# Optimization experiments

Hardware: AMD Instinct MI355X
Metric: run time of the kernel (lower is better)

Reference implementation:

```python
import jax, jax.numpy as jnp
import numpy as np

E = 1024
H = 16
HD = E // H


def setup_inputs() -> dict:
    key = jax.random.key(0)
    k1, k2, k3, k4, k5 = jax.random.split(key, 5)
    x = jax.random.normal(k1, (2, 2048, E), dtype=jnp.float32)
    s = 1.0 / np.sqrt(E)
    qkv_w = jax.random.uniform(k2, (3 * E, E), jnp.float32, -s, s)
    qkv_b = jax.random.uniform(k3, (3 * E,), jnp.float32, -s, s)
    o_w = jax.random.uniform(k4, (E, E), jnp.float32, -s, s)
    o_b = jax.random.uniform(k5, (E,), jnp.float32, -s, s)
    return {"x": x, "qkv_w": qkv_w, "qkv_b": qkv_b, "o_w": o_w, "o_b": o_b}


def reference(x, qkv_w, qkv_b, o_w, o_b):
    B, T, _ = x.shape
    # qkv projection (torch Linear: x @ W.T + b)
    qkv = x @ qkv_w.T + qkv_b  # [B,T,3E]
    q, k, v = jnp.split(qkv, 3, axis=-1)
    # [B,H,T,HD]
    q = q.reshape(B, T, H, HD).transpose(0, 2, 1, 3)
    k = k.reshape(B, T, H, HD).transpose(0, 2, 1, 3)
    v = v.reshape(B, T, H, HD).transpose(0, 2, 1, 3)
    scores = jnp.einsum('bhqd,bhkd->bhqk', q, k) / np.sqrt(HD)
    causal = jnp.tril(jnp.ones((T, T), dtype=bool))
    scores = jnp.where(causal, scores, -jnp.inf)
    attn = jax.nn.softmax(scores, axis=-1)  # dropout disabled (eval mode)
    y = jnp.einsum('bhqk,bhkd->bhqd', attn, v)
    y = y.transpose(0, 2, 1, 3).reshape(B, T, E)
    return y @ o_w.T + o_b
```

## Files before the change

### kernel.cpp

```cpp
#include <hip/hip_runtime.h>
#include <hip/hip_bf16.h>
#include <math.h>

#define BATCH 2
#define SEQ   2048
#define EMB   1024
#define NH    16
#define HD    64
#define M_ROWS (BATCH * SEQ)

typedef __attribute__((ext_vector_type(8))) short bf16x8;
typedef __attribute__((ext_vector_type(4))) float f32x4;

__device__ __forceinline__ ushort f2bf(float f) {
    unsigned u = __float_as_uint(f);
    unsigned lsb = (u >> 16) & 1u;
    u += 0x7fffu + lsb;
    return (ushort)(u >> 16);
}

__device__ __forceinline__ unsigned cvt_pk_bf16(float lo, float hi) {
    unsigned r;
    asm("v_cvt_pk_bf16_f32 %0, %1, %2" : "=v"(r) : "v"(lo), "v"(hi));
    return r;
}

__device__ __forceinline__ void gload_lds16(const void* g, void* l) {
    __builtin_amdgcn_global_load_lds(
        (const __attribute__((address_space(1))) unsigned int*)g,
        (__attribute__((address_space(3))) unsigned int*)l, 16, 0, 0);
}

__global__ __launch_bounds__(256) void cvt3_f32_bf16(
    const float* __restrict__ s1, const float* __restrict__ s2,
    const float* __restrict__ s3, ushort* __restrict__ out,
    int n1, int n2)
{
    int i = (blockIdx.x * 256 + threadIdx.x) * 4;
    const float* src;
    int off;
    if (i < n1)            { src = s1; off = i; }
    else if (i < n1 + n2)  { src = s2; off = i - n1; }
    else                   { src = s3; off = i - n1 - n2; }
    float4 v = *reinterpret_cast<const float4*>(&src[off]);
    uint2 pk;
    pk.x = cvt_pk_bf16(v.x, v.y);
    pk.y = cvt_pk_bf16(v.z, v.w);
    *reinterpret_cast<uint2*>(&out[i]) = pk;
}

template <int MODE>
__global__ __launch_bounds__(256) void gemm_mfma_abt(
    const ushort* __restrict__ A, const ushort* __restrict__ B,
    const float* __restrict__ bias, float* __restrict__ Cout,
    ushort* __restrict__ qkb, ushort* __restrict__ vtb,
    int M, int N, int K)
{
    __shared__ ushort Al[128 * 64];
    __shared__ ushort Bl[128 * 64];

    const int tid  = threadIdx.x;
    const int lane = tid & 63;
    const int wave = tid >> 6;
    const int wr   = wave >> 1;
    const int wc   = wave & 1;
    const int l15  = lane & 15;
    const int l4   = lane >> 4;
    const int m0   = blockIdx.y * 128;
    const int n0   = blockIdx.x * 128;

    f32x4 acc[4][4];
#pragma unroll
    for (int m = 0; m < 4; ++m)
#pragma unroll
        for (int n = 0; n < 4; ++n)
#pragma unroll
            for (int r = 0; r < 4; ++r) acc[m][n][r] = 0.f;

    for (int k0 = 0; k0 < K; k0 += 64) {
#pragma unroll
        for (int it = 0; it < 4; ++it) {
            int chunk = tid + it * 256;
            int row = chunk >> 3;
            int kc  = (chunk & 7) * 8;
            gload_lds16(&A[(size_t)(m0 + row) * K + k0 + kc], &Al[chunk * 8]);
            gload_lds16(&B[(size_t)(n0 + row) * K + k0 + kc], &Bl[chunk * 8]);
        }
        __syncthreads();

#pragma unroll
        for (int kk = 0; kk < 2; ++kk) {
            const int ko = kk * 32 + l4 * 8;
            bf16x8 a[4], b[4];
#pragma unroll
            for (int m = 0; m < 4; ++m)
                a[m] = *reinterpret_cast<const bf16x8*>(
                    &Al[(wr * 64 + m * 16 + l15) * 64 + ko]);
#pragma unroll
            for (int n = 0; n < 4; ++n)
                b[n] = *reinterpret_cast<const bf16x8*>(
                    &Bl[(wc * 64 + n * 16 + l15) * 64 + ko]);
            __builtin_amdgcn_s_setprio(1);
#pragma unroll
            for (int m = 0; m < 4; ++m)
#pragma unroll
                for (int n = 0; n < 4; ++n)
                    acc[m][n] = __builtin_amdgcn_mfma_f32_16x16x32_bf16(
                        a[m], b[n], acc[m][n], 0, 0, 0);
            __builtin_amdgcn_s_setprio(0);
        }
        __syncthreads();
    }

#pragma unroll
    for (int n = 0; n < 4; ++n) {
        const int col = n0 + wc * 64 + n * 16 + l15;
        const float bv = bias[col];
        if (MODE == 0) {
#pragma unroll
            for (int m = 0; m < 4; ++m) {
                const int row0 = m0 + wr * 64 + m * 16 + l4 * 4;
#pragma unroll
                for (int r = 0; r < 4; ++r)
                    Cout[(size_t)(row0 + r) * N + col] = acc[m][n][r] + bv;
            }
        } else if (col < 2 * EMB) {
#pragma unroll
            for (int m = 0; m < 4; ++m) {
                const int row0 = m0 + wr * 64 + m * 16 + l4 * 4;
#pragma unroll
                for (int r = 0; r < 4; ++r)
                    qkb[(size_t)(row0 + r) * 2048 + col] = f2bf(acc[m][n][r] + bv);
            }
        } else {
            const int h = (col - 2 * EMB) >> 6;
            const int d = col & 63;
#pragma unroll
            for (int m = 0; m < 4; ++m) {
                const int row0 = m0 + wr * 64 + m * 16 + l4 * 4;
                const int bb = row0 >> 11;
                const int t  = row0 & 2047;
                uint2 pk;
                pk.x = cvt_pk_bf16(acc[m][n][0] + bv, acc[m][n][1] + bv);
                pk.y = cvt_pk_bf16(acc[m][n][2] + bv, acc[m][n][3] + bv);
                *reinterpret_cast<uint2*>(
                    &vtb[((size_t)(bb * 16 + h) * 64 + d) * 2048 + t]) = pk;
            }
        }
    }
}

__global__ __launch_bounds__(256) void attn_mfma(
    const ushort* __restrict__ qk, const ushort* __restrict__ vt,
    ushort* __restrict__ y)
{
    __shared__ alignas(16) ushort Kl[4][4096];
    __shared__ alignas(16) ushort Vl[4][4096];
    __shared__ alignas(16) ushort QP[8192];

    const int tid  = threadIdx.x;
    const int lane = tid & 63;
    const int w    = tid >> 6;
    const int l15  = lane & 15;
    const int l4   = lane >> 4;

    const int id  = blockIdx.x;
    const int xcd = id & 7;
    const int s   = (id >> 3) & 15;
    const int g   = id >> 7;
    const int bh  = xcd * 4 + g;
    const int qt  = (g < 2) ? (15 - s) : s;
    const int b   = bh >> 4;
    const int h   = bh & 15;

    const ushort* qbase = qk + (size_t)b * SEQ * 2048 + h * HD;
    const ushort* kbase = qbase + EMB;
    const ushort* vbase = vt + (size_t)bh * HD * SEQ;

    const int swz   = (l15 & 7) << 4;
    const int koff0 = ((l4 * 16) ^ swz) >> 1;
    const int koff1 = ((64 + l4 * 16) ^ swz) >> 1;

#pragma unroll
    for (int it = 0; it < 4; ++it) {
        int i = tid + it * 256;
        int r = i >> 3;
        int c = ((i & 7) ^ (r & 7)) << 3;
        gload_lds16(qbase + (size_t)(qt * 128 + r) * 2048 + c, &QP[i * 8]);
    }
#pragma unroll
    for (int it = 0; it < 2; ++it) {
        int i = tid + it * 256;
        int r = i >> 3;
        int c = ((i & 7) ^ (r & 7)) << 3;
        gload_lds16(kbase + (size_t)r * 2048 + c, &Kl[0][i * 8]);
        gload_lds16(kbase + (size_t)(64 + r) * 2048 + c, &Kl[1][i * 8]);
    }
#pragma unroll
    for (int it = 0; it < 2; ++it) {
        int i = tid + it * 256;
        int d = i >> 3;
        int c = ((i & 7) ^ (d & 7)) << 3;
        gload_lds16(vbase + (size_t)d * 2048 + c, &Vl[0][i * 8]);
        gload_lds16(vbase + (size_t)d * 2048 + 64 + c, &Vl[1][i * 8]);
    }
    __syncthreads();

    const int qrow0 = (w * 32 + l15) * 64;
    const int qrow1 = (w * 32 + 16 + l15) * 64;
    const bf16x8 qf00 = *reinterpret_cast<const bf16x8*>(&QP[qrow0 + koff0]);
    const bf16x8 qf01 = *reinterpret_cast<const bf16x8*>(&QP[qrow0 + koff1]);
    const bf16x8 qf10 = *reinterpret_cast<const bf16x8*>(&QP[qrow1 + koff0]);
    const bf16x8 qf11 = *reinterpret_cast<const bf16x8*>(&QP[qrow1 + koff1]);

    int pso[4];
#pragma unroll
    for (int n = 0; n < 4; ++n) pso[n] = ((n * 32 + l4 * 8) ^ swz) >> 1;

    const short OBF = (short)0x3F80;
    const bf16x8 ones = {OBF, OBF, OBF, OBF, OBF, OBF, OBF, OBF};

    f32x4 o0[4], o1[4];
#pragma unroll
    for (int n = 0; n < 4; ++n)
#pragma unroll
        for (int r = 0; r < 4; ++r) { o0[n][r] = 0.f; o1[n][r] = 0.f; }
    f32x4 lacc0 = {0.f, 0.f, 0.f, 0.f};
    f32x4 lacc1 = {0.f, 0.f, 0.f, 0.f};
    float m0 = -3.0e38f;
    float m1 = -3.0e38f;

    const float BETA = 0.18033688f;
    const int nkv = 2 * qt + 2;

    auto computeTile = [&](const ushort* Kb, const ushort* Vb, int kkt) {
        bf16x8 kf[4][2];
#pragma unroll
        for (int n = 0; n < 4; ++n) {
            kf[n][0] = *reinterpret_cast<const bf16x8*>(
                &Kb[(n * 16 + l15) * 64 + koff0]);
            kf[n][1] = *reinterpret_cast<const bf16x8*>(
                &Kb[(n * 16 + l15) * 64 + koff1]);
        }
        f32x4 s0[4], s1[4];
        __builtin_amdgcn_s_setprio(1);
#pragma unroll
        for (int n = 0; n < 4; ++n) {
            f32x4 z0 = {0.f, 0.f, 0.f, 0.f};
            z0 = __builtin_amdgcn_mfma_f32_16x16x32_bf16(kf[n][0], qf00, z0, 0, 0, 0);
            s0[n] = __builtin_amdgcn_mfma_f32_16x16x32_bf16(kf[n][1], qf01, z0, 0, 0, 0);
            f32x4 z1 = {0.f, 0.f, 0.f, 0.f};
            z1 = __builtin_amdgcn_mfma_f32_16x16x32_bf16(kf[n][0], qf10, z1, 0, 0, 0);
            s1[n] = __builtin_amdgcn_mfma_f32_16x16x32_bf16(kf[n][1], qf11, z1, 0, 0, 0);
        }
        __builtin_amdgcn_s_setprio(0);

        bf16x8 vf[4][2];
#pragma unroll
        for (int n = 0; n < 4; ++n) {
            vf[n][0] = *reinterpret_cast<const bf16x8*>(
                &Vb[(n * 16 + l15) * 64 + koff0]);
            vf[n][1] = *reinterpret_cast<const bf16x8*>(
                &Vb[(n * 16 + l15) * 64 + koff1]);
        }

        if (kkt >= nkv - 2) {
            const int q0 = qt * 128 + w * 32 + l15;
            const int q1 = q0 + 16;
#pragma unroll
            for (int n = 0; n < 4; ++n)
#pragma unroll
                for (int r = 0; r < 4; ++r) {
                    int kg = kkt * 64 + n * 16 + l4 * 4 + r;
                    if (kg > q0) s0[n][r] = -3.0e38f;
                    if (kg > q1) s1[n][r] = -3.0e38f;
                }
        }

        float pm0, pm1;
        {
            float a0 = fmaxf(fmaxf(s0[0][0], s0[0][1]), fmaxf(s0[0][2], s0[0][3]));
            float a1 = fmaxf(fmaxf(s0[1][0], s0[1][1]), fmaxf(s0[1][2], s0[1][3]));
            float a2 = fmaxf(fmaxf(s0[2][0], s0[2][1]), fmaxf(s0[2][2], s0[2][3]));
            float a3 = fmaxf(fmaxf(s0[3][0], s0[3][1]), fmaxf(s0[3][2], s0[3][3]));
            pm0 = fmaxf(fmaxf(a0, a1), fmaxf(a2, a3)) * BETA;
            float b0 = fmaxf(fmaxf(s1[0][0], s1[0][1]), fmaxf(s1[0][2], s1[0][3]));
            float b1 = fmaxf(fmaxf(s1[1][0], s1[1][1]), fmaxf(s1[1][2], s1[1][3]));
            float b2 = fmaxf(fmaxf(s1[2][0], s1[2][1]), fmaxf(s1[2][2], s1[2][3]));
            float b3 = fmaxf(fmaxf(s1[3][0], s1[3][1]), fmaxf(s1[3][2], s1[3][3]));
            pm1 = fmaxf(fmaxf(b0, b1), fmaxf(b2, b3)) * BETA;
        }

        if (__any((pm0 > m0 + 8.0f) || (pm1 > m1 + 8.0f))) {
            float tm0 = fmaxf(pm0, __shfl_xor(pm0, 16));
            tm0 = fmaxf(tm0, __shfl_xor(tm0, 32));
            float tm1 = fmaxf(pm1, __shfl_xor(pm1, 16));
            tm1 = fmaxf(tm1, __shfl_xor(tm1, 32));
            float mn0 = fmaxf(m0, tm0);
            float al0 = exp2f(m0 - mn0);
            m0 = mn0;
            float mn1 = fmaxf(m1, tm1);
            float al1 = exp2f(m1 - mn1);
            m1 = mn1;
            float a00 = __shfl(al0, l4 * 4 + 0, 16);
            float a01 = __shfl(al0, l4 * 4 + 1, 16);
            float a02 = __shfl(al0, l4 * 4 + 2, 16);
            float a03 = __shfl(al0, l4 * 4 + 3, 16);
            float a10 = __shfl(al1, l4 * 4 + 0, 16);
            float a11 = __shfl(al1, l4 * 4 + 1, 16);
            float a12 = __shfl(al1, l4 * 4 + 2, 16);
            float a13 = __shfl(al1, l4 * 4 + 3, 16);
            lacc0[0] *= a00; lacc0[1] *= a01; lacc0[2] *= a02; lacc0[3] *= a03;
            lacc1[0] *= a10; lacc1[1] *= a11; lacc1[2] *= a12; lacc1[3] *= a13;
#pragma unroll
            for (int n = 0; n < 4; ++n) {
                o0[n][0] *= a00; o0[n][1] *= a01; o0[n][2] *= a02; o0[n][3] *= a03;
                o1[n][0] *= a10; o1[n][1] *= a11; o1[n][2] *= a12; o1[n][3] *= a13;
            }
        }

#pragma unroll
        for (int n = 0; n < 4; ++n) {
            float pa = exp2f(fmaf(s0[n][0], BETA, -m0));
            float pb = exp2f(fmaf(s0[n][1], BETA, -m0));
            float pc = exp2f(fmaf(s0[n][2], BETA, -m0));
            float pd = exp2f(fmaf(s0[n][3], BETA, -m0));
            uint2 pk;
            pk.x = cvt_pk_bf16(pa, pb);
            pk.y = cvt_pk_bf16(pc, pd);
            *reinterpret_cast<uint2*>(&QP[qrow0 + pso[n]]) = pk;
            pa = exp2f(fmaf(s1[n][0], BETA, -m1));
            pb = exp2f(fmaf(s1[n][1], BETA, -m1));
            pc = exp2f(fmaf(s1[n][2], BETA, -m1));
            pd = exp2f(fmaf(s1[n][3], BETA, -m1));
            pk.x = cvt_pk_bf16(pa, pb);
            pk.y = cvt_pk_bf16(pc, pd);
            *reinterpret_cast<uint2*>(&QP[qrow1 + pso[n]]) = pk;
        }

        bf16x8 pf00 = *reinterpret_cast<const bf16x8*>(&QP[qrow0 + koff0]);
        bf16x8 pf01 = *reinterpret_cast<const bf16x8*>(&QP[qrow0 + koff1]);
        bf16x8 pf10 = *reinterpret_cast<const bf16x8*>(&QP[qrow1 + koff0]);
        bf16x8 pf11 = *reinterpret_cast<const bf16x8*>(&QP[qrow1 + koff1]);
        __builtin_amdgcn_s_setprio(1);
        lacc0 = __builtin_amdgcn_mfma_f32_16x16x32_bf16(pf00, ones, lacc0, 0, 0, 0);
        lacc0 = __builtin_amdgcn_mfma_f32_16x16x32_bf16(pf01, ones, lacc0, 0, 0, 0);
        lacc1 = __builtin_amdgcn_mfma_f32_16x16x32_bf16(pf10, ones, lacc1, 0, 0, 0);
        lacc1 = __builtin_amdgcn_mfma_f32_16x16x32_bf16(pf11, ones, lacc1, 0, 0, 0);
#pragma unroll
        for (int n = 0; n < 4; ++n) {
            o0[n] = __builtin_amdgcn_mfma_f32_16x16x32_bf16(pf00, vf[n][0], o0[n], 0, 0, 0);
            o0[n] = __builtin_amdgcn_mfma_f32_16x16x32_bf16(pf01, vf[n][1], o0[n], 0, 0, 0);
            o1[n] = __builtin_amdgcn_mfma_f32_16x16x32_bf16(pf10, vf[n][0], o1[n], 0, 0, 0);
            o1[n] = __builtin_amdgcn_mfma_f32_16x16x32_bf16(pf11, vf[n][1], o1[n], 0, 0, 0);
        }
        __builtin_amdgcn_s_setprio(0);
    };

    for (int kk = 0; kk < nkv; kk += 2) {
        if (kk + 2 < nkv) {
            const int b2 = (kk + 2) & 3;
            const int b3 = (kk + 3) & 3;
#pragma unroll
            for (int it = 0; it < 2; ++it) {
                int i = tid + it * 256;
                int r = i >> 3;
                int c = ((i & 7) ^ (r & 7)) << 3;
                gload_lds16(kbase + (size_t)((kk + 2) * 64 + r) * 2048 + c,
                            &Kl[b2][i * 8]);
                gload_lds16(kbase + (size_t)((kk + 3) * 64 + r) * 2048 + c,
                            &Kl[b3][i * 8]);
            }
#pragma unroll
            for (int it = 0; it < 2; ++it) {
                int i = tid + it * 256;
                int d = i >> 3;
                int c = ((i & 7) ^ (d & 7)) << 3;
                gload_lds16(vbase + (size_t)d * 2048 + (kk + 2) * 64 + c,
                            &Vl[b2][i * 8]);
                gload_lds16(vbase + (size_t)d * 2048 + (kk + 3) * 64 + c,
                            &Vl[b3][i * 8]);
            }
        }

        computeTile(Kl[kk & 3], Vl[kk & 3], kk);
        computeTile(Kl[(kk + 1) & 3], Vl[(kk + 1) & 3], kk + 1);
        __syncthreads();
    }

#pragma unroll
    for (int r = 0; r < 4; ++r) {
        float inv0 = 1.f / lacc0[r];
        float inv1 = 1.f / lacc1[r];
        int row0 = qt * 128 + w * 32 + l4 * 4 + r;
        int row1 = row0 + 16;
#pragma unroll
        for (int n = 0; n < 4; ++n) {
            y[(size_t)(b * SEQ + row0) * EMB + h * HD + n * 16 + l15] =
                f2bf(o0[n][r] * inv0);
            y[(size_t)(b * SEQ + row1) * EMB + h * HD + n * 16 + l15] =
                f2bf(o1[n][r] * inv1);
        }
    }
}

extern "C" void kernel_launch(void* const* d_in, const int* in_sizes, int n_in,
                              void* d_out, int out_size, void* d_ws, size_t ws_size,
                              hipStream_t stream)
{
    const float* x     = (const float*)d_in[0];
    const float* qkv_w = (const float*)d_in[1];
    const float* qkv_b = (const float*)d_in[2];
    const float* o_w   = (const float*)d_in[3];
    const float* o_b   = (const float*)d_in[4];
    float* out = (float*)d_out;

    ushort* xb    = (ushort*)d_ws;
    ushort* wqkvb = xb    + (size_t)M_ROWS * EMB;
    ushort* owb   = wqkvb + (size_t)3 * EMB * EMB;
    ushort* qkb   = owb   + (size_t)EMB * EMB;
    ushort* vtb   = qkb   + (size_t)M_ROWS * 2 * EMB;
    ushort* ybb   = vtb   + (size_t)32 * HD * SEQ;

    {
        int n1 = M_ROWS * EMB;
        int n2 = 3 * EMB * EMB;
        int ntot = n1 + n2 + EMB * EMB;
        cvt3_f32_bf16<<<ntot / 1024, 256, 0, stream>>>(
            x, qkv_w, o_w, xb, n1, n2);
    }

    {
        dim3 grid(3 * EMB / 128, M_ROWS / 128);
        gemm_mfma_abt<1><<<grid, 256, 0, stream>>>(
            xb, wqkvb, qkv_b, nullptr, qkb, vtb, M_ROWS, 3 * EMB, EMB);
    }

    {
        attn_mfma<<<512, 256, 0, stream>>>(qkb, vtb, ybb);
    }

    {
        dim3 grid(EMB / 128, M_ROWS / 128);
        gemm_mfma_abt<0><<<grid, 256, 0, stream>>>(
            ybb, owb, o_b, out, nullptr, nullptr, M_ROWS, EMB, EMB);
    }
}
```

Before: 129.2 us.

## Use 512-thread attention blocks that each process a paired light and heavy query tile

The attention kernel now launches 256 blocks of 512 threads instead of 512 blocks of 256. Each wave owns 16 query rows rather than 32, and each block runs two passes over query tiles pp and 15-pp, so every block does the same total causal work. The aim is to balance causal work across blocks and get more waves per block to hide latency. In exchange, each wave has half the MFMA work per K/V tile, the two passes run back to back, and block-wide barriers now span 8 waves.

```diff
diff --git a/kernel.cpp b/kernel.cpp
--- a/kernel.cpp
+++ b/kernel.cpp
@@ -150,7 +150,7 @@
     }
 }
 
-__global__ __launch_bounds__(256) void attn_mfma(
+__global__ __launch_bounds__(512) void attn_mfma(
     const ushort* __restrict__ qk, const ushort* __restrict__ vt,
     ushort* __restrict__ y)
 {
@@ -166,10 +166,8 @@
 
     const int id  = blockIdx.x;
     const int xcd = id & 7;
-    const int s   = (id >> 3) & 15;
-    const int g   = id >> 7;
-    const int bh  = xcd * 4 + g;
-    const int qt  = (g < 2) ? (15 - s) : s;
+    const int bh  = xcd * 4 + ((id >> 3) & 3);
+    const int pp  = id >> 5;
     const int b   = bh >> 4;
     const int h   = bh & 15;
 
@@ -181,226 +179,162 @@
     const int koff0 = ((l4 * 16) ^ swz) >> 1;
     const int koff1 = ((64 + l4 * 16) ^ swz) >> 1;
 
-#pragma unroll
-    for (int it = 0; it < 4; ++it) {
-        int i = tid + it * 256;
-        int r = i >> 3;
-        int c = ((i & 7) ^ (r & 7)) << 3;
-        gload_lds16(qbase + (size_t)(qt * 128 + r) * 2048 + c, &QP[i * 8]);
-    }
-#pragma unroll
-    for (int it = 0; it < 2; ++it) {
-        int i = tid + it * 256;
-        int r = i >> 3;
-        int c = ((i & 7) ^ (r & 7)) << 3;
-        gload_lds16(kbase + (size_t)r * 2048 + c, &Kl[0][i * 8]);
-        gload_lds16(kbase + (size_t)(64 + r) * 2048 + c, &Kl[1][i * 8]);
-    }
-#pragma unroll
-    for (int it = 0; it < 2; ++it) {
-        int i = tid + it * 256;
-        int d = i >> 3;
-        int c = ((i & 7) ^ (d & 7)) << 3;
-        gload_lds16(vbase + (size_t)d * 2048 + c, &Vl[0][i * 8]);
-        gload_lds16(vbase + (size_t)d * 2048 + 64 + c, &Vl[1][i * 8]);
-    }
-    __syncthreads();
-
-    const int qrow0 = (w * 32 + l15) * 64;
-    const int qrow1 = (w * 32 + 16 + l15) * 64;
-    const bf16x8 qf00 = *reinterpret_cast<const bf16x8*>(&QP[qrow0 + koff0]);
-    const bf16x8 qf01 = *reinterpret_cast<const bf16x8*>(&QP[qrow0 + koff1]);
-    const bf16x8 qf10 = *reinterpret_cast<const bf16x8*>(&QP[qrow1 + koff0]);
-    const bf16x8 qf11 = *reinterpret_cast<const bf16x8*>(&QP[qrow1 + koff1]);
-
     int pso[4];
 #pragma unroll
     for (int n = 0; n < 4; ++n) pso[n] = ((n * 32 + l4 * 8) ^ swz) >> 1;
 
     const short OBF = (short)0x3F80;
     const bf16x8 ones = {OBF, OBF, OBF, OBF, OBF, OBF, OBF, OBF};
-
-    f32x4 o0[4], o1[4];
-#pragma unroll
-    for (int n = 0; n < 4; ++n)
-#pragma unroll
-        for (int r = 0; r < 4; ++r) { o0[n][r] = 0.f; o1[n][r] = 0.f; }
-    f32x4 lacc0 = {0.f, 0.f, 0.f, 0.f};
-    f32x4 lacc1 = {0.f, 0.f, 0.f, 0.f};
-    float m0 = -3.0e38f;
-    float m1 = -3.0e38f;
-
     const float BETA = 0.18033688f;
-    const int nkv = 2 * qt + 2;
-
-    auto computeTile = [&](const ushort* Kb, const ushort* Vb, int kkt) {
-        bf16x8 kf[4][2];
-#pragma unroll
-        for (int n = 0; n < 4; ++n) {
-            kf[n][0] = *reinterpret_cast<const bf16x8*>(
-                &Kb[(n * 16 + l15) * 64 + koff0]);
-            kf[n][1] = *reinterpret_cast<const bf16x8*>(
-                &Kb[(n * 16 + l15) * 64 + koff1]);
-        }
-        f32x4 s0[4], s1[4];
-        __builtin_amdgcn_s_setprio(1);
-#pragma unroll
-        for (int n = 0; n < 4; ++n) {
-            f32x4 z0 = {0.f, 0.f, 0.f, 0.f};
-            z0 = __builtin_amdgcn_mfma_f32_16x16x32_bf16(kf[n][0], qf00, z0, 0, 0, 0);
-            s0[n] = __builtin_amdgcn_mfma_f32_16x16x32_bf16(kf[n][1], qf01, z0, 0, 0, 0);
-            f32x4 z1 = {0.f, 0.f, 0.f, 0.f};
-            z1 = __builtin_amdgcn_mfma_f32_16x16x32_bf16(kf[n][0], qf10, z1, 0, 0, 0);
-            s1[n] = __builtin_amdgcn_mfma_f32_16x16x32_bf16(kf[n][1], qf11, z1, 0, 0, 0);
-        }
-        __builtin_amdgcn_s_setprio(0);
-
-        bf16x8 vf[4][2];
-#pragma unroll
-        for (int n = 0; n < 4; ++n) {
-            vf[n][0] = *reinterpret_cast<const bf16x8*>(
-                &Vb[(n * 16 + l15) * 64 + koff0]);
-            vf[n][1] = *reinterpret_cast<const bf16x8*>(
-                &Vb[(n * 16 + l15) * 64 + koff1]);
-        }
-
-        if (kkt >= nkv - 2) {
-            const int q0 = qt * 128 + w * 32 + l15;
-            const int q1 = q0 + 16;
-#pragma unroll
-            for (int n = 0; n < 4; ++n)
-#pragma unroll
-                for (int r = 0; r < 4; ++r) {
-                    int kg = kkt * 64 + n * 16 + l4 * 4 + r;
-                    if (kg > q0) s0[n][r] = -3.0e38f;
-                    if (kg > q1) s1[n][r] = -3.0e38f;
+
+    const int qrow = (w * 16 + l15) * 64;
+
+    const int sr = tid >> 3;
+    const int sc = ((tid & 7) ^ (sr & 7)) << 3;
+    const int i2 = tid + 512;
+    const int qr2 = i2 >> 3;
+    const int qc2 = ((i2 & 7) ^ (qr2 & 7)) << 3;
+
+#pragma unroll
+    for (int pass = 0; pass < 2; ++pass) {
+        const int qt  = pass ? (15 - pp) : pp;
+        const int nkv = 2 * qt + 2;
+
+        gload_lds16(qbase + (size_t)(qt * 128 + sr) * 2048 + sc, &QP[tid * 8]);
+        gload_lds16(qbase + (size_t)(qt * 128 + qr2) * 2048 + qc2, &QP[i2 * 8]);
+        gload_lds16(kbase + (size_t)sr * 2048 + sc, &Kl[0][tid * 8]);
+        gload_lds16(kbase + (size_t)(64 + sr) * 2048 + sc, &Kl[1][tid * 8]);
+        gload_lds16(vbase + (size_t)sr * 2048 + sc, &Vl[0][tid * 8]);
+        gload_lds16(vbase + (size_t)sr * 2048 + 64 + sc, &Vl[1][tid * 8]);
+        __syncthreads();
+
+        const bf16x8 qf0 = *reinterpret_cast<const bf16x8*>(&QP[qrow + koff0]);
+        const bf16x8 qf1 = *reinterpret_cast<const bf16x8*>(&QP[qrow + koff1]);
+
+        f32x4 o[4];
+#pragma unroll
+        for (int n = 0; n < 4; ++n)
+#pragma unroll
+            for (int r = 0; r < 4; ++r) o[n][r] = 0.f;
+        f32x4 lacc = {0.f, 0.f, 0.f, 0.f};
+        float m = -3.0e38f;
+
+        auto computeTile = [&](const ushort* Kb, const ushort* Vb, int kkt) {
+            bf16x8 kf[4][2];
+#pragma unroll
+            for (int n = 0; n < 4; ++n) {
+                kf[n][0] = *reinterpret_cast<const bf16x8*>(
+                    &Kb[(n * 16 + l15) * 64 + koff0]);
+                kf[n][1] = *reinterpret_cast<const bf16x8*>(
+                    &Kb[(n * 16 + l15) * 64 + koff1]);
+            }
+            f32x4 s[4];
+            __builtin_amdgcn_s_setprio(1);
+#pragma unroll
+            for (int n = 0; n < 4; ++n) {
+                f32x4 z = {0.f, 0.f, 0.f, 0.f};
+                z = __builtin_amdgcn_mfma_f32_16x16x32_bf16(kf[n][0], qf0, z, 0, 0, 0);
+                s[n] = __builtin_amdgcn_mfma_f32_16x16x32_bf16(kf[n][1], qf1, z, 0, 0, 0);
+            }
+            __builtin_amdgcn_s_setprio(0);
+
+            bf16x8 vf[4][2];
+#pragma unroll
+            for (int n = 0; n < 4; ++n) {
+                vf[n][0] = *reinterpret_cast<const bf16x8*>(
+                    &Vb[(n * 16 + l15) * 64 + koff0]);
+                vf[n][1] = *reinterpret_cast<const bf16x8*>(
+                    &Vb[(n * 16 + l15) * 64 + koff1]);
+            }
+
+            if (kkt >= nkv - 2) {
+                const int q0 = qt * 128 + w * 16 + l15;
+#pragma unroll
+                for (int n = 0; n < 4; ++n)
+#pragma unroll
+                    for (int r = 0; r < 4; ++r) {
+                        int kg = kkt * 64 + n * 16 + l4 * 4 + r;
+                        if (kg > q0) s[n][r] = -3.0e38f;
+                    }
+            }
+
+            float a0 = fmaxf(fmaxf(s[0][0], s[0][1]), fmaxf(s[0][2], s[0][3]));
+            float a1 = fmaxf(fmaxf(s[1][0], s[1][1]), fmaxf(s[1][2], s[1][3]));
+            float a2 = fmaxf(fmaxf(s[2][0], s[2][1]), fmaxf(s[2][2], s[2][3]));
+            float a3 = fmaxf(fmaxf(s[3][0], s[3][1]), fmaxf(s[3][2], s[3][3]));
+            float pm = fmaxf(fmaxf(a0, a1), fmaxf(a2, a3)) * BETA;
+
+            if (__any(pm > m + 8.0f)) {
+                float tm = fmaxf(pm, __shfl_xor(pm, 16));
+                tm = fmaxf(tm, __shfl_xor(tm, 32));
+                float mn = fmaxf(m, tm);
+                float al = exp2f(m - mn);
+                m = mn;
+                float b0 = __shfl(al, l4 * 4 + 0, 16);
+                float b1 = __shfl(al, l4 * 4 + 1, 16);
+                float b2 = __shfl(al, l4 * 4 + 2, 16);
+                float b3 = __shfl(al, l4 * 4 + 3, 16);
+                lacc[0] *= b0; lacc[1] *= b1; lacc[2] *= b2; lacc[3] *= b3;
+#pragma unroll
+                for (int n = 0; n < 4; ++n) {
+                    o[n][0] *= b0; o[n][1] *= b1; o[n][2] *= b2; o[n][3] *= b3;
                 }
-        }
-
-        float pm0, pm1;
-        {
-            float a0 = fmaxf(fmaxf(s0[0][0], s0[0][1]), fmaxf(s0[0][2], s0[0][3]));
-            float a1 = fmaxf(fmaxf(s0[1][0], s0[1][1]), fmaxf(s0[1][2], s0[1][3]));
-            float a2 = fmaxf(fmaxf(s0[2][0], s0[2][1]), fmaxf(s0[2][2], s0[2][3]));
-            float a3 = fmaxf(fmaxf(s0[3][0], s0[3][1]), fmaxf(s0[3][2], s0[3][3]));
-            pm0 = fmaxf(fmaxf(a0, a1), fmaxf(a2, a3)) * BETA;
-            float b0 = fmaxf(fmaxf(s1[0][0], s1[0][1]), fmaxf(s1[0][2], s1[0][3]));
-            float b1 = fmaxf(fmaxf(s1[1][0], s1[1][1]), fmaxf(s1[1][2], s1[1][3]));
-            float b2 = fmaxf(fmaxf(s1[2][0], s1[2][1]), fmaxf(s1[2][2], s1[2][3]));
-            float b3 = fmaxf(fmaxf(s1[3][0], s1[3][1]), fmaxf(s1[3][2], s1[3][3]));
-            pm1 = fmaxf(fmaxf(b0, b1), fmaxf(b2, b3)) * BETA;
-        }
-
-        if (__any((pm0 > m0 + 8.0f) || (pm1 > m1 + 8.0f))) {
-            float tm0 = fmaxf(pm0, __shfl_xor(pm0, 16));
-            tm0 = fmaxf(tm0, __shfl_xor(tm0, 32));
-            float tm1 = fmaxf(pm1, __shfl_xor(pm1, 16));
-            tm1 = fmaxf(tm1, __shfl_xor(tm1, 32));
-            float mn0 = fmaxf(m0, tm0);
-            float al0 = exp2f(m0 - mn0);
-            m0 = mn0;
-            float mn1 = fmaxf(m1, tm1);
-            float al1 = exp2f(m1 - mn1);
-            m1 = mn1;
-            float a00 = __shfl(al0, l4 * 4 + 0, 16);
-            float a01 = __shfl(al0, l4 * 4 + 1, 16);
-            float a02 = __shfl(al0, l4 * 4 + 2, 16);
-            float a03 = __shfl(al0, l4 * 4 + 3, 16);
-            float a10 = __shfl(al1, l4 * 4 + 0, 16);
-            float a11 = __shfl(al1, l4 * 4 + 1, 16);
-            float a12 = __shfl(al1, l4 * 4 + 2, 16);
-            float a13 = __shfl(al1, l4 * 4 + 3, 16);
-            lacc0[0] *= a00; lacc0[1] *= a01; lacc0[2] *= a02; lacc0[3] *= a03;
-            lacc1[0] *= a10; lacc1[1] *= a11; lacc1[2] *= a12; lacc1[3] *= a13;
-#pragma unroll
-            for (int n = 0; n < 4; ++n) {
-                o0[n][0] *= a00; o0[n][1] *= a01; o0[n][2] *= a02; o0[n][3] *= a03;
-                o1[n][0] *= a10; o1[n][1] *= a11; o1[n][2] *= a12; o1[n][3] *= a13;
-            }
-        }
-
-#pragma unroll
-        for (int n = 0; n < 4; ++n) {
-            float pa = exp2f(fmaf(s0[n][0], BETA, -m0));
-            float pb = exp2f(fmaf(s0[n][1], BETA, -m0));
-            float pc = exp2f(fmaf(s0[n][2], BETA, -m0));
-            float pd = exp2f(fmaf(s0[n][3], BETA, -m0));
-            uint2 pk;
-            pk.x = cvt_pk_bf16(pa, pb);
-            pk.y = cvt_pk_bf16(pc, pd);
-            *reinterpret_cast<uint2*>(&QP[qrow0 + pso[n]]) = pk;
-            pa = exp2f(fmaf(s1[n][0], BETA, -m1));
-            pb = exp2f(fmaf(s1[n][1], BETA, -m1));
-            pc = exp2f(fmaf(s1[n][2], BETA, -m1));
-            pd = exp2f(fmaf(s1[n][3], BETA, -m1));
-            pk.x = cvt_pk_bf16(pa, pb);
-            pk.y = cvt_pk_bf16(pc, pd);
-            *reinterpret_cast<uint2*>(&QP[qrow1 + pso[n]]) = pk;
-        }
-
-        bf16x8 pf00 = *reinterpret_cast<const bf16x8*>(&QP[qrow0 + koff0]);
-        bf16x8 pf01 = *reinterpret_cast<const bf16x8*>(&QP[qrow0 + koff1]);
-        bf16x8 pf10 = *reinterpret_cast<const bf16x8*>(&QP[qrow1 + koff0]);
-        bf16x8 pf11 = *reinterpret_cast<const bf16x8*>(&QP[qrow1 + koff1]);
-        __builtin_amdgcn_s_setprio(1);
-        lacc0 = __builtin_amdgcn_mfma_f32_16x16x32_bf16(pf00, ones, lacc0, 0, 0, 0);
-        lacc0 = __builtin_amdgcn_mfma_f32_16x16x32_bf16(pf01, ones, lacc0, 0, 0, 0);
-        lacc1 = __builtin_amdgcn_mfma_f32_16x16x32_bf16(pf10, ones, lacc1, 0, 0, 0);
-        lacc1 = __builtin_amdgcn_mfma_f32_16x16x32_bf16(pf11, ones, lacc1, 0, 0, 0);
-#pragma unroll
-        for (int n = 0; n < 4; ++n) {
-            o0[n] = __builtin_amdgcn_mfma_f32_16x16x32_bf16(pf00, vf[n][0], o0[n], 0, 0, 0);
-            o0[n] = __builtin_amdgcn_mfma_f32_16x16x32_bf16(pf01, vf[n][1], o0[n], 0, 0, 0);
-            o1[n] = __builtin_amdgcn_mfma_f32_16x16x32_bf16(pf10, vf[n][0], o1[n], 0, 0, 0);
-            o1[n] = __builtin_amdgcn_mfma_f32_16x16x32_bf16(pf11, vf[n][1], o1[n], 0, 0, 0);
-        }
-        __builtin_amdgcn_s_setprio(0);
-    };
-
-    for (int kk = 0; kk < nkv; kk += 2) {
-        if (kk + 2 < nkv) {
-            const int b2 = (kk + 2) & 3;
-            const int b3 = (kk + 3) & 3;
-#pragma unroll
-            for (int it = 0; it < 2; ++it) {
-                int i = tid + it * 256;
-                int r = i >> 3;
-                int c = ((i & 7) ^ (r & 7)) << 3;
-                gload_lds16(kbase + (size_t)((kk + 2) * 64 + r) * 2048 + c,
-                            &Kl[b2][i * 8]);
-                gload_lds16(kbase + (size_t)((kk + 3) * 64 + r) * 2048 + c,
-                            &Kl[b3][i * 8]);
-            }
-#pragma unroll
-            for (int it = 0; it < 2; ++it) {
-                int i = tid + it * 256;
-                int d = i >> 3;
-                int c = ((i & 7) ^ (d & 7)) << 3;
-                gload_lds16(vbase + (size_t)d * 2048 + (kk + 2) * 64 + c,
-                            &Vl[b2][i * 8]);
-                gload_lds16(vbase + (size_t)d * 2048 + (kk + 3) * 64 + c,
-                            &Vl[b3][i * 8]);
-            }
-        }
-
-        computeTile(Kl[kk & 3], Vl[kk & 3], kk);
-        computeTile(Kl[(kk + 1) & 3], Vl[(kk + 1) & 3], kk + 1);
+            }
+
+#pragma unroll
+            for (int n = 0; n < 4; ++n) {
+                float pa = exp2f(fmaf(s[n][0], BETA, -m));
+                float pb = exp2f(fmaf(s[n][1], BETA, -m));
+                float pc = exp2f(fmaf(s[n][2], BETA, -m));
+                float pd = exp2f(fmaf(s[n][3], BETA, -m));
+                uint2 pk;
+                pk.x = cvt_pk_bf16(pa, pb);
+                pk.y = cvt_pk_bf16(pc, pd);
+                *reinterpret_cast<uint2*>(&QP[qrow + pso[n]]) = pk;
+            }
+
+            bf16x8 pf0 = *reinterpret_cast<const bf16x8*>(&QP[qrow + koff0]);
+            bf16x8 pf1 = *reinterpret_cast<const bf16x8*>(&QP[qrow + koff1]);
+            __builtin_amdgcn_s_setprio(1);
+            lacc = __builtin_amdgcn_mfma_f32_16x16x32_bf16(pf0, ones, lacc, 0, 0, 0);
+            lacc = __builtin_amdgcn_mfma_f32_16x16x32_bf16(pf1, ones, lacc, 0, 0, 0);
+#pragma unroll
+            for (int n = 0; n < 4; ++n) {
+                o[n] = __builtin_amdgcn_mfma_f32_16x16x32_bf16(pf0, vf[n][0], o[n], 0, 0, 0);
+                o[n] = __builtin_amdgcn_mfma_f32_16x16x32_bf16(pf1, vf[n][1], o[n], 0, 0, 0);
+            }
+            __builtin_amdgcn_s_setprio(0);
+        };
+
+        for (int kk = 0; kk < nkv; kk += 2) {
+            if (kk + 2 < nkv) {
+                const int b2 = (kk + 2) & 3;
+                const int b3 = (kk + 3) & 3;
+                gload_lds16(kbase + (size_t)((kk + 2) * 64 + sr) * 2048 + sc,
+                            &Kl[b2][tid * 8]);
+                gload_lds16(kbase + (size_t)((kk + 3) * 64 + sr) * 2048 + sc,
+                            &Kl[b3][tid * 8]);
+                gload_lds16(vbase + (size_t)sr * 2048 + (kk + 2) * 64 + sc,
+                            &Vl[b2][tid * 8]);
+                gload_lds16(vbase + (size_t)sr * 2048 + (kk + 3) * 64 + sc,
+                            &Vl[b3][tid * 8]);
+            }
+            computeTile(Kl[kk & 3], Vl[kk & 3], kk);
+            computeTile(Kl[(kk + 1) & 3], Vl[(kk + 1) & 3], kk + 1);
+            __syncthreads();
+        }
+
+#pragma unroll
+        for (int r = 0; r < 4; ++r) {
+            float inv = 1.f / lacc[r];
+            int row = qt * 128 + w * 16 + l4 * 4 + r;
+#pragma unroll
+            for (int n = 0; n < 4; ++n) {
+                y[(size_t)(b * SEQ + row) * EMB + h * HD + n * 16 + l15] =
+                    f2bf(o[n][r] * inv);
+            }
+        }
         __syncthreads();
-    }
-
-#pragma unroll
-    for (int r = 0; r < 4; ++r) {
-        float inv0 = 1.f / lacc0[r];
-        float inv1 = 1.f / lacc1[r];
-        int row0 = qt * 128 + w * 32 + l4 * 4 + r;
-        int row1 = row0 + 16;
-#pragma unroll
-        for (int n = 0; n < 4; ++n) {
-            y[(size_t)(b * SEQ + row0) * EMB + h * HD + n * 16 + l15] =
-                f2bf(o0[n][r] * inv0);
-            y[(size_t)(b * SEQ + row1) * EMB + h * HD + n * 16 + l15] =
-                f2bf(o1[n][r] * inv1);
-        }
     }
 }
 
@@ -437,7 +371,7 @@
     }
 
     {
-        attn_mfma<<<512, 256, 0, stream>>>(qkb, vtb, ybb);
+        attn_mfma<<<256, 512, 0, stream>>>(qkb, vtb, ybb);
     }
 
     {
```

After: 113.7 us. -12.0%, faster.

## Pair mirrored causal query tiles in one block sharing K/V loads, prescale Q

Applied to the files above, without the earlier changes.

The attention kernel now runs 512-thread blocks where two groups of four waves handle a query tile and its mirrored partner (pp and 15-pp). Both groups share the same K/V LDS stream, so each K/V tile is loaded once for two query tiles and every block has balanced causal work. Waves skip tiles beyond their causal limit, including the last half tile for some waves. The softmax scale (1/sqrt(d)·log2e) is folded into Q in the QKV GEMM epilogue, which removes per-element FMAs in the inner loop. The trade-offs are one extra bf16 rounding on the scaled Q, half as many blocks in the grid, and idle waves in the diagonal tiles.

```diff
diff --git a/kernel.cpp b/kernel.cpp
--- a/kernel.cpp
+++ b/kernel.cpp
@@ -125,12 +125,14 @@
                     Cout[(size_t)(row0 + r) * N + col] = acc[m][n][r] + bv;
             }
         } else if (col < 2 * EMB) {
+            const float qs = (col < EMB) ? 0.18033688f : 1.0f;
 #pragma unroll
             for (int m = 0; m < 4; ++m) {
                 const int row0 = m0 + wr * 64 + m * 16 + l4 * 4;
 #pragma unroll
                 for (int r = 0; r < 4; ++r)
-                    qkb[(size_t)(row0 + r) * 2048 + col] = f2bf(acc[m][n][r] + bv);
+                    qkb[(size_t)(row0 + r) * 2048 + col] =
+                        f2bf((acc[m][n][r] + bv) * qs);
             }
         } else {
             const int h = (col - 2 * EMB) >> 6;
@@ -150,28 +152,32 @@
     }
 }
 
-__global__ __launch_bounds__(256) void attn_mfma(
+__global__ __launch_bounds__(512) void attn_mfma(
     const ushort* __restrict__ qk, const ushort* __restrict__ vt,
     ushort* __restrict__ y)
 {
     __shared__ alignas(16) ushort Kl[4][4096];
     __shared__ alignas(16) ushort Vl[4][4096];
-    __shared__ alignas(16) ushort QP[8192];
+    __shared__ alignas(16) ushort QP[16384];
 
     const int tid  = threadIdx.x;
     const int lane = tid & 63;
     const int w    = tid >> 6;
+    const int u    = w & 3;
+    const int wg   = w >> 2;
     const int l15  = lane & 15;
     const int l4   = lane >> 4;
 
     const int id  = blockIdx.x;
     const int xcd = id & 7;
-    const int s   = (id >> 3) & 15;
-    const int g   = id >> 7;
-    const int bh  = xcd * 4 + g;
-    const int qt  = (g < 2) ? (15 - s) : s;
+    const int bh  = xcd * 4 + ((id >> 3) & 3);
+    const int pp  = id >> 5;
     const int b   = bh >> 4;
     const int h   = bh & 15;
+
+    const int qtX  = wg ? (15 - pp) : pp;
+    const int nkvX = 2 * qtX + 2;
+    const int nkvM = 32 - 2 * pp;
 
     const ushort* qbase = qk + (size_t)b * SEQ * 2048 + h * HD;
     const ushort* kbase = qbase + EMB;
@@ -180,46 +186,38 @@
     const int swz   = (l15 & 7) << 4;
     const int koff0 = ((l4 * 16) ^ swz) >> 1;
     const int koff1 = ((64 + l4 * 16) ^ swz) >> 1;
+    int pso[4];
+#pragma unroll
+    for (int n = 0; n < 4; ++n) pso[n] = ((n * 32 + l4 * 8) ^ swz) >> 1;
+
+    const short OBF = (short)0x3F80;
+    const bf16x8 ones = {OBF, OBF, OBF, OBF, OBF, OBF, OBF, OBF};
+
+    const int qrow0 = (wg * 128 + u * 32 + l15) * 64;
+    const int qrow1 = qrow0 + 16 * 64;
+
+    const int sr = tid >> 3;
+    const int sc = ((tid & 7) ^ (sr & 7)) << 3;
 
 #pragma unroll
     for (int it = 0; it < 4; ++it) {
-        int i = tid + it * 256;
-        int r = i >> 3;
-        int c = ((i & 7) ^ (r & 7)) << 3;
-        gload_lds16(qbase + (size_t)(qt * 128 + r) * 2048 + c, &QP[i * 8]);
-    }
-#pragma unroll
-    for (int it = 0; it < 2; ++it) {
-        int i = tid + it * 256;
-        int r = i >> 3;
-        int c = ((i & 7) ^ (r & 7)) << 3;
-        gload_lds16(kbase + (size_t)r * 2048 + c, &Kl[0][i * 8]);
-        gload_lds16(kbase + (size_t)(64 + r) * 2048 + c, &Kl[1][i * 8]);
-    }
-#pragma unroll
-    for (int it = 0; it < 2; ++it) {
-        int i = tid + it * 256;
-        int d = i >> 3;
-        int c = ((i & 7) ^ (d & 7)) << 3;
-        gload_lds16(vbase + (size_t)d * 2048 + c, &Vl[0][i * 8]);
-        gload_lds16(vbase + (size_t)d * 2048 + 64 + c, &Vl[1][i * 8]);
-    }
+        int c = tid + it * 512;
+        int r256 = c >> 3;
+        int cc = ((c & 7) ^ (r256 & 7)) << 3;
+        int grow = ((r256 >> 7) ? (15 - pp) : pp) * 128 + (r256 & 127);
+        gload_lds16(qbase + (size_t)grow * 2048 + cc, &QP[c * 8]);
+    }
+    gload_lds16(kbase + (size_t)sr * 2048 + sc, &Kl[0][tid * 8]);
+    gload_lds16(kbase + (size_t)(64 + sr) * 2048 + sc, &Kl[1][tid * 8]);
+    gload_lds16(vbase + (size_t)sr * 2048 + sc, &Vl[0][tid * 8]);
+    gload_lds16(vbase + (size_t)sr * 2048 + 64 + sc, &Vl[1][tid * 8]);
     __syncthreads();
 
-    const int qrow0 = (w * 32 + l15) * 64;
-    const int qrow1 = (w * 32 + 16 + l15) * 64;
     const bf16x8 qf00 = *reinterpret_cast<const bf16x8*>(&QP[qrow0 + koff0]);
     const bf16x8 qf01 = *reinterpret_cast<const bf16x8*>(&QP[qrow0 + koff1]);
     const bf16x8 qf10 = *reinterpret_cast<const bf16x8*>(&QP[qrow1 + koff0]);
     const bf16x8 qf11 = *reinterpret_cast<const bf16x8*>(&QP[qrow1 + koff1]);
 
-    int pso[4];
-#pragma unroll
-    for (int n = 0; n < 4; ++n) pso[n] = ((n * 32 + l4 * 8) ^ swz) >> 1;
-
-    const short OBF = (short)0x3F80;
-    const bf16x8 ones = {OBF, OBF, OBF, OBF, OBF, OBF, OBF, OBF};
-
     f32x4 o0[4], o1[4];
 #pragma unroll
     for (int n = 0; n < 4; ++n)
@@ -227,11 +225,10 @@
         for (int r = 0; r < 4; ++r) { o0[n][r] = 0.f; o1[n][r] = 0.f; }
     f32x4 lacc0 = {0.f, 0.f, 0.f, 0.f};
     f32x4 lacc1 = {0.f, 0.f, 0.f, 0.f};
-    float m0 = -3.0e38f;
-    float m1 = -3.0e38f;
-
-    const float BETA = 0.18033688f;
-    const int nkv = 2 * qt + 2;
+    float m0 = -3.0e38f, m1 = -3.0e38f;
+
+    const int q0g = qtX * 128 + u * 32 + l15;
+    const int q1g = q0g + 16;
 
     auto computeTile = [&](const ushort* Kb, const ushort* Vb, int kkt) {
         bf16x8 kf[4][2];
@@ -264,32 +261,27 @@
                 &Vb[(n * 16 + l15) * 64 + koff1]);
         }
 
-        if (kkt >= nkv - 2) {
-            const int q0 = qt * 128 + w * 32 + l15;
-            const int q1 = q0 + 16;
+        if (kkt >= nkvX - 2) {
 #pragma unroll
             for (int n = 0; n < 4; ++n)
 #pragma unroll
                 for (int r = 0; r < 4; ++r) {
                     int kg = kkt * 64 + n * 16 + l4 * 4 + r;
-                    if (kg > q0) s0[n][r] = -3.0e38f;
-                    if (kg > q1) s1[n][r] = -3.0e38f;
+                    if (kg > q0g) s0[n][r] = -3.0e38f;
+                    if (kg > q1g) s1[n][r] = -3.0e38f;
                 }
         }
 
-        float pm0, pm1;
-        {
-            float a0 = fmaxf(fmaxf(s0[0][0], s0[0][1]), fmaxf(s0[0][2], s0[0][3]));
-            float a1 = fmaxf(fmaxf(s0[1][0], s0[1][1]), fmaxf(s0[1][2], s0[1][3]));
-            float a2 = fmaxf(fmaxf(s0[2][0], s0[2][1]), fmaxf(s0[2][2], s0[2][3]));
-            float a3 = fmaxf(fmaxf(s0[3][0], s0[3][1]), fmaxf(s0[3][2], s0[3][3]));
-            pm0 = fmaxf(fmaxf(a0, a1), fmaxf(a2, a3)) * BETA;
-            float b0 = fmaxf(fmaxf(s1[0][0], s1[0][1]), fmaxf(s1[0][2], s1[0][3]));
-            float b1 = fmaxf(fmaxf(s1[1][0], s1[1][1]), fmaxf(s1[1][2], s1[1][3]));
-            float b2 = fmaxf(fmaxf(s1[2][0], s1[2][1]), fmaxf(s1[2][2], s1[2][3]));
-            float b3 = fmaxf(fmaxf(s1[3][0], s1[3][1]), fmaxf(s1[3][2], s1[3][3]));
-            pm1 = fmaxf(fmaxf(b0, b1), fmaxf(b2, b3)) * BETA;
-        }
+        float pa0 = fmaxf(fmaxf(s0[0][0], s0[0][1]), fmaxf(s0[0][2], s0[0][3]));
+        float pa1 = fmaxf(fmaxf(s0[1][0], s0[1][1]), fmaxf(s0[1][2], s0[1][3]));
+        float pa2 = fmaxf(fmaxf(s0[2][0], s0[2][1]), fmaxf(s0[2][2], s0[2][3]));
+        float pa3 = fmaxf(fmaxf(s0[3][0], s0[3][1]), fmaxf(s0[3][2], s0[3][3]));
+        float pm0 = fmaxf(fmaxf(pa0, pa1), fmaxf(pa2, pa3));
+        float pb0 = fmaxf(fmaxf(s1[0][0], s1[0][1]), fmaxf(s1[0][2], s1[0][3]));
+        float pb1 = fmaxf(fmaxf(s1[1][0], s1[1][1]), fmaxf(s1[1][2], s1[1][3]));
+        float pb2 = fmaxf(fmaxf(s1[2][0], s1[2][1]), fmaxf(s1[2][2], s1[2][3]));
+        float pb3 = fmaxf(fmaxf(s1[3][0], s1[3][1]), fmaxf(s1[3][2], s1[3][3]));
+        float pm1 = fmaxf(fmaxf(pb0, pb1), fmaxf(pb2, pb3));
 
         if (__any((pm0 > m0 + 8.0f) || (pm1 > m1 + 8.0f))) {
             float tm0 = fmaxf(pm0, __shfl_xor(pm0, 16));
@@ -321,18 +313,18 @@
 
 #pragma unroll
         for (int n = 0; n < 4; ++n) {
-            float pa = exp2f(fmaf(s0[n][0], BETA, -m0));
-            float pb = exp2f(fmaf(s0[n][1], BETA, -m0));
-            float pc = exp2f(fmaf(s0[n][2], BETA, -m0));
-            float pd = exp2f(fmaf(s0[n][3], BETA, -m0));
+            float pa = exp2f(s0[n][0] - m0);
+            float pb = exp2f(s0[n][1] - m0);
+            float pc = exp2f(s0[n][2] - m0);
+            float pd = exp2f(s0[n][3] - m0);
             uint2 pk;
             pk.x = cvt_pk_bf16(pa, pb);
             pk.y = cvt_pk_bf16(pc, pd);
             *reinterpret_cast<uint2*>(&QP[qrow0 + pso[n]]) = pk;
-            pa = exp2f(fmaf(s1[n][0], BETA, -m1));
-            pb = exp2f(fmaf(s1[n][1], BETA, -m1));
-            pc = exp2f(fmaf(s1[n][2], BETA, -m1));
-            pd = exp2f(fmaf(s1[n][3], BETA, -m1));
+            pa = exp2f(s1[n][0] - m1);
+            pb = exp2f(s1[n][1] - m1);
+            pc = exp2f(s1[n][2] - m1);
+            pd = exp2f(s1[n][3] - m1);
             pk.x = cvt_pk_bf16(pa, pb);
             pk.y = cvt_pk_bf16(pc, pd);
             *reinterpret_cast<uint2*>(&QP[qrow1 + pso[n]]) = pk;
@@ -357,34 +349,27 @@
         __builtin_amdgcn_s_setprio(0);
     };
 
-    for (int kk = 0; kk < nkv; kk += 2) {
-        if (kk + 2 < nkv) {
+    auto doTile = [&](int t) {
+        if (t >= nkvX) return;
+        if (t == nkvX - 1 && u < 2) return;
+        computeTile(Kl[t & 3], Vl[t & 3], t);
+    };
+
+    for (int kk = 0; kk < nkvM; kk += 2) {
+        if (kk + 2 < nkvM) {
             const int b2 = (kk + 2) & 3;
             const int b3 = (kk + 3) & 3;
-#pragma unroll
-            for (int it = 0; it < 2; ++it) {
-                int i = tid + it * 256;
-                int r = i >> 3;
-                int c = ((i & 7) ^ (r & 7)) << 3;
-                gload_lds16(kbase + (size_t)((kk + 2) * 64 + r) * 2048 + c,
-                            &Kl[b2][i * 8]);
-                gload_lds16(kbase + (size_t)((kk + 3) * 64 + r) * 2048 + c,
-                            &Kl[b3][i * 8]);
-            }
-#pragma unroll
-            for (int it = 0; it < 2; ++it) {
-                int i = tid + it * 256;
-                int d = i >> 3;
-                int c = ((i & 7) ^ (d & 7)) << 3;
-                gload_lds16(vbase + (size_t)d * 2048 + (kk + 2) * 64 + c,
-                            &Vl[b2][i * 8]);
-                gload_lds16(vbase + (size_t)d * 2048 + (kk + 3) * 64 + c,
-                            &Vl[b3][i * 8]);
-            }
-        }
-
-        computeTile(Kl[kk & 3], Vl[kk & 3], kk);
-        computeTile(Kl[(kk + 1) & 3], Vl[(kk + 1) & 3], kk + 1);
+            gload_lds16(kbase + (size_t)((kk + 2) * 64 + sr) * 2048 + sc,
+                        &Kl[b2][tid * 8]);
+            gload_lds16(kbase + (size_t)((kk + 3) * 64 + sr) * 2048 + sc,
+                        &Kl[b3][tid * 8]);
+            gload_lds16(vbase + (size_t)sr * 2048 + (kk + 2) * 64 + sc,
+                        &Vl[b2][tid * 8]);
+            gload_lds16(vbase + (size_t)sr * 2048 + (kk + 3) * 64 + sc,
+                        &Vl[b3][tid * 8]);
+        }
+        doTile(kk);
+        doTile(kk + 1);
         __syncthreads();
     }
 
@@ -392,7 +377,7 @@
     for (int r = 0; r < 4; ++r) {
         float inv0 = 1.f / lacc0[r];
         float inv1 = 1.f / lacc1[r];
-        int row0 = qt * 128 + w * 32 + l4 * 4 + r;
+        int row0 = qtX * 128 + u * 32 + l4 * 4 + r;
         int row1 = row0 + 16;
 #pragma unroll
         for (int n = 0; n < 4; ++n) {
@@ -437,7 +422,7 @@
     }
 
     {
-        attn_mfma<<<512, 256, 0, stream>>>(qkb, vtb, ybb);
+        attn_mfma<<<256, 512, 0, stream>>>(qkb, vtb, ybb);
     }
 
     {
```

Result: faster. 119.0 us (-7.9%).
